# Kernel optimization log

Measured on AMD Instinct MI355X. Metric: run time of the kernel, lower is better.

## Reference

```python
import jax, jax.numpy as jnp
import numpy as np

N = 100000   # nodes
E = 200000   # edges
L = 3        # GNN layers
D = 300      # node feature dim
H = 150      # per-direction message dim


def setup_inputs() -> dict:
    key = jax.random.key(0)
    ks = jax.random.split(key, 8)
    s = 0.05
    return {
        "x": jax.random.normal(ks[0], (N, D), jnp.float32),
        "edge_index": jax.random.randint(ks[1], (2, E), 0, N, dtype=jnp.int32),
        "Wr": jax.random.normal(ks[2], (L, 2 * D, H), jnp.float32) * s,
        "br": jax.random.normal(ks[3], (L, H), jnp.float32) * s,
        "Wc": jax.random.normal(ks[4], (L, 2 * D, H), jnp.float32) * s,
        "bc": jax.random.normal(ks[5], (L, H), jnp.float32) * s,
        "Wa": jax.random.normal(ks[6], (D, D), jnp.float32) * s,
        "ba": jax.random.normal(ks[7], (D,), jnp.float32) * s,
    }


def _gelu(z):
    return jax.nn.gelu(z, approximate=False)  # torch GELU is exact erf


def _msg_aggr(v, src, dst, W, b):
    # message at each edge: GELU(Linear(cat(x_i, x_j))), x_i = target, x_j = source
    m = _gelu(jnp.concatenate([v[dst], v[src]], axis=-1) @ W + b)  # [E, H]
    # sum-aggregate messages at target nodes
    return jax.ops.segment_sum(m, dst, num_segments=N)  # [N, H]


def reference(x, edge_index, Wr, br, Wc, bc, Wa, ba):
    src, dst = edge_index[0], edge_index[1]

    def step(v, p):
        Wr_l, br_l, Wc_l, bc_l = p
        r = _msg_aggr(v, src, dst, Wr_l, br_l)        # r2c: original direction
        c = _msg_aggr(v, dst, src, Wc_l, bc_l)        # c2r: flipped edge_index
        v = v + _gelu(jnp.concatenate([r, c], axis=-1) @ Wa + ba)
        return v, None

    out, _ = jax.lax.scan(step, x, (Wr, br, Wc, bc))
    return out
```

## Files before the change

kernel.cpp:

```cpp
#include <hip/hip_runtime.h>
#include <hip/hip_bf16.h>
#include <math.h>

#define NND 100000
#define EE  200000
#define LL  3
#define DD  300
#define HH  150

#define MPAD 100096
#define KP   320
#define NPJ  640
#define NUP  384
#define NTK  (KP / 32)

#define NB   49
#define SCN  (NB * 2048)

typedef __attribute__((ext_vector_type(8))) short bf16x8;
typedef __attribute__((ext_vector_type(4))) short bf16x4;
typedef __attribute__((ext_vector_type(4))) float f32x4;

__device__ __forceinline__ float gelu_exact(float z) {
    return 0.5f * z * (1.0f + erff(z * 0.7071067811865475f));
}
__device__ __forceinline__ unsigned short f2bf(float f) {
    union { float fv; unsigned u; } v; v.fv = f;
    unsigned r = v.u + 0x7fff + ((v.u >> 16) & 1);
    return (unsigned short)(r >> 16);
}
__device__ __forceinline__ float bf2f(unsigned short b) {
    union { unsigned u; float fv; } v; v.u = ((unsigned)b) << 16;
    return v.fv;
}

__global__ __launch_bounds__(256) void pack_w(
    const float* __restrict__ Wr, const float* __restrict__ Wc,
    const float* __restrict__ Wa,
    unsigned short* __restrict__ Bt, unsigned short* __restrict__ Wat)
{
    int i = blockIdx.x * 256 + threadIdx.x;
    const int btTotal = LL * NPJ * KP;
    if (i < btTotal) {
        int l = i / (NPJ * KP);
        int rem = i % (NPJ * KP);
        int n = rem / KP;
        int k = rem % KP;
        float v = 0.f;
        if (k < DD && n < 600) {
            const float* W = (n < 300) ? Wr : Wc;
            int nn = (n < 300) ? n : n - 300;
            int krow = (nn < 150) ? k : 300 + k;
            int j    = (nn < 150) ? nn : nn - 150;
            v = W[(size_t)l * 600 * 150 + (size_t)krow * 150 + j];
        }
        Bt[i] = f2bf(v);
    } else {
        int i2 = i - btTotal;
        if (i2 < NUP * KP) {
            int n = i2 / KP, k = i2 % KP;
            float v = (n < DD && k < DD) ? Wa[(size_t)k * DD + n] : 0.f;
            Wat[i2] = f2bf(v);
        }
    }
}

__global__ __launch_bounds__(256) void init_vbf(
    const float* __restrict__ x, unsigned short* __restrict__ vbf)
{
    int idx = blockIdx.x * 256 + threadIdx.x;
    int row = idx / (KP / 8);
    int gk  = (idx % (KP / 8)) * 8;
    if (row >= MPAD) return;
    unsigned short tmp[8];
    if (row < NND && gk < DD) {
        if (gk + 8 <= DD) {
            const float4* p = (const float4*)(x + (size_t)row * DD + gk);
            float4 f0 = p[0], f1 = p[1];
            tmp[0] = f2bf(f0.x); tmp[1] = f2bf(f0.y);
            tmp[2] = f2bf(f0.z); tmp[3] = f2bf(f0.w);
            tmp[4] = f2bf(f1.x); tmp[5] = f2bf(f1.y);
            tmp[6] = f2bf(f1.z); tmp[7] = f2bf(f1.w);
        } else {
            #pragma unroll
            for (int j = 0; j < 8; ++j)
                tmp[j] = (gk + j < DD) ? f2bf(x[(size_t)row * DD + gk + j]) : 0;
        }
    } else {
        #pragma unroll
        for (int j = 0; j < 8; ++j) tmp[j] = 0;
    }
    *((bf16x8*)&vbf[(size_t)row * KP + gk]) = *((bf16x8*)tmp);
}

__global__ __launch_bounds__(256) void hist_deg(
    const int* __restrict__ src, const int* __restrict__ dst,
    int* __restrict__ deg)
{
    int e = blockIdx.x * 256 + threadIdx.x;
    if (e >= EE) return;
    atomicAdd(&deg[dst[e]], 1);
    atomicAdd(&deg[SCN + src[e]], 1);
}

__global__ __launch_bounds__(256) void scanA(
    const int* __restrict__ deg, int* __restrict__ off, int* __restrict__ bsum)
{
    __shared__ int ls[256];
    const int t = threadIdx.x, row = blockIdx.y;
    const int base = blockIdx.x * 2048 + t * 8;
    const int* dg = deg + (size_t)row * SCN + base;
    int v[8];
    #pragma unroll
    for (int j = 0; j < 8; ++j) v[j] = dg[j];
    int tot = 0;
    #pragma unroll
    for (int j = 0; j < 8; ++j) tot += v[j];
    ls[t] = tot;
    __syncthreads();
    #pragma unroll
    for (int d = 1; d < 256; d <<= 1) {
        int tv = (t >= d) ? ls[t - d] : 0;
        __syncthreads();
        ls[t] += tv;
        __syncthreads();
    }
    int run = ls[t] - tot;
    int* op = off + (size_t)row * SCN + base;
    #pragma unroll
    for (int j = 0; j < 8; ++j) { op[j] = run; run += v[j]; }
    if (t == 255) bsum[row * 64 + blockIdx.x] = ls[255];
}

__global__ __launch_bounds__(256) void scanB(int* __restrict__ bsum)
{
    if (threadIdx.x < 2) {
        int row = threadIdx.x, c = 0;
        for (int i = 0; i < NB; ++i) {
            int tv = bsum[row * 64 + i];
            bsum[row * 64 + i] = c;
            c += tv;
        }
    }
}

__global__ __launch_bounds__(256) void scanC(
    int* __restrict__ off, const int* __restrict__ bsum, int* __restrict__ cur)
{
    const int t = threadIdx.x, row = blockIdx.y;
    const int base = blockIdx.x * 2048 + t * 8;
    const int add = bsum[row * 64 + blockIdx.x];
    int* op = off + (size_t)row * SCN + base;
    int* cp = cur + (size_t)row * SCN + base;
    #pragma unroll
    for (int j = 0; j < 8; ++j) {
        int v = op[j] + add;
        op[j] = v;
        cp[j] = v;
    }
}

__global__ __launch_bounds__(256) void fill_adj(
    const int* __restrict__ src, const int* __restrict__ dst,
    int* __restrict__ cur, int* __restrict__ adj)
{
    int e = blockIdx.x * 256 + threadIdx.x;
    if (e >= EE) return;
    int s = src[e], d = dst[e];
    int pd = atomicAdd(&cur[d], 1);
    adj[pd] = s;
    int ps = atomicAdd(&cur[SCN + s], 1);
    adj[EE + ps] = d;
}

__global__ __launch_bounds__(256) void aggregate(
    const int* __restrict__ off, const int* __restrict__ adj,
    const unsigned short* __restrict__ P,
    const float* __restrict__ br, const float* __restrict__ bc,
    unsigned short* __restrict__ RC)
{
    const int n    = blockIdx.x * 4 + (threadIdx.x >> 6);
    const int dir  = blockIdx.y;
    const int lane = threadIdx.x & 63;
    const int h0 = lane, h1 = lane + 64, h2 = lane + 128;

    unsigned short* outrow = RC + (size_t)n * KP + dir * 150;
    if (n >= NND) {
        outrow[h0] = 0; outrow[h1] = 0;
        if (h2 < (dir ? 170 : 150)) outrow[h2] = 0;
        return;
    }

    const int* offp = off + (size_t)dir * SCN;
    const int* adjp = adj + (size_t)dir * EE;
    const float* bias = dir ? bc : br;
    const unsigned short* own = P + (size_t)n * NPJ + dir * 300;
    const int poff = dir ? 450 : 150;

    float o0 = bf2f(own[h0]) + bias[h0];
    float o1 = bf2f(own[h1]) + bias[h1];
    float o2 = (h2 < 150) ? bf2f(own[h2]) + bias[h2] : 0.f;

    float s0 = 0.f, s1 = 0.f, s2 = 0.f;
    int beg = offp[n], end = offp[n + 1];
    for (int i = beg; i < end; ++i) {
        const unsigned short* pp = P + (size_t)adjp[i] * NPJ + poff;
        s0 += gelu_exact(o0 + bf2f(pp[h0]));
        s1 += gelu_exact(o1 + bf2f(pp[h1]));
        if (h2 < 150) s2 += gelu_exact(o2 + bf2f(pp[h2]));
    }
    outrow[h0] = f2bf(s0);
    outrow[h1] = f2bf(s1);
    if (h2 < 150)                  outrow[h2] = f2bf(s2);
    else if (dir == 1 && h2 < 170) outrow[h2] = 0;
}

#define GLOAD16(gp, lp) __builtin_amdgcn_global_load_lds( \
    (const __attribute__((address_space(1))) unsigned int*)(gp), \
    (__attribute__((address_space(3))) unsigned int*)(lp), 16, 0, 0)

#define STAGE_LDS(dstp, srcbase, rowoff, k0) do {                            \
    _Pragma("unroll")                                                        \
    for (int i_ = 0; i_ < 2; ++i_) {                                         \
        int cb_ = wid * 128 + i_ * 64;                                       \
        int ci_ = cb_ + lane;                                                \
        int row_ = ci_ >> 2, pc_ = ci_ & 3;                                  \
        int c_ = pc_ ^ ((row_ >> 1) & 3);                                    \
        GLOAD16(srcbase + (size_t)(rowoff + row_) * KP + (k0) + c_ * 8,      \
                &(dstp)[cb_ * 8]);                                           \
    } } while (0)

template<int MODE>
__global__ __launch_bounds__(256) void gemm_mfma(
    const unsigned short* __restrict__ Ab,
    const unsigned short* __restrict__ Bt,
    unsigned short* __restrict__ P,
    float* __restrict__ outv, unsigned short* __restrict__ vbf,
    const float* __restrict__ bias, int last)
{
    __shared__ char smem[49152];
    float* bounce = (float*)smem;

    const int tid  = threadIdx.x;
    const int lane = tid & 63;
    const int wid  = tid >> 6;

    const int gx   = gridDim.x;
    const int nwg  = gx * gridDim.y;
    const int flat = blockIdx.y * gx + blockIdx.x;
    const int q = nwg >> 3, r = nwg & 7;
    const int xcd = flat & 7, off = flat >> 3;
    const int lid = (xcd < r ? xcd * (q + 1) : r * (q + 1) + (xcd - r) * q) + off;
    const int brow = (lid / gx) * 128;
    const int bcol = (lid % gx) * 128;

    const int wm = (wid >> 1) * 64;
    const int wn = (wid & 1) * 64;

    f32x4 acc[4][4];
    #pragma unroll
    for (int i = 0; i < 4; ++i)
        #pragma unroll
        for (int j = 0; j < 4; ++j)
            #pragma unroll
            for (int rr = 0; rr < 4; ++rr) acc[i][j][rr] = 0.f;

    #pragma unroll
    for (int t = 0; t < 2; ++t) {
        unsigned short* Al = (unsigned short*)(smem + t * 16384);
        unsigned short* Bl = (unsigned short*)(smem + t * 16384 + 8192);
        STAGE_LDS(Al, Ab, brow, t * 32);
        STAGE_LDS(Bl, Bt, bcol, t * 32);
    }

    #pragma unroll
    for (int t = 0; t < NTK; ++t) {
        const int b  = t % 3;
        unsigned short* Alc = (unsigned short*)(smem + b * 16384);
        unsigned short* Blc = (unsigned short*)(smem + b * 16384 + 8192);
        if (t + 2 < NTK) {
            const int bn = (t + 2) % 3;
            unsigned short* Aln = (unsigned short*)(smem + bn * 16384);
            unsigned short* Bln = (unsigned short*)(smem + bn * 16384 + 8192);
            STAGE_LDS(Aln, Ab, brow, (t + 2) * 32);
            STAGE_LDS(Bln, Bt, bcol, (t + 2) * 32);
            asm volatile("s_waitcnt vmcnt(8)" ::: "memory");
        } else if (t + 1 < NTK) {
            asm volatile("s_waitcnt vmcnt(4)" ::: "memory");
        } else {
            asm volatile("s_waitcnt vmcnt(0)" ::: "memory");
        }
        __builtin_amdgcn_s_barrier();

        bf16x8 af[4], bfr[4];
        #pragma unroll
        for (int mi = 0; mi < 4; ++mi) {
            int row = wm + mi * 16 + (lane & 15);
            af[mi] = *((const bf16x8*)&Alc[row * 32 + (((lane >> 4) ^ ((row >> 1) & 3)) * 8)]);
        }
        #pragma unroll
        for (int nj = 0; nj < 4; ++nj) {
            int row = wn + nj * 16 + (lane & 15);
            bfr[nj] = *((const bf16x8*)&Blc[row * 32 + (((lane >> 4) ^ ((row >> 1) & 3)) * 8)]);
        }
        __builtin_amdgcn_s_setprio(1);
        #pragma unroll
        for (int mi = 0; mi < 4; ++mi)
            #pragma unroll
            for (int nj = 0; nj < 4; ++nj)
                acc[mi][nj] = __builtin_amdgcn_mfma_f32_16x16x32_bf16(
                    af[mi], bfr[nj], acc[mi][nj], 0, 0, 0);
        __builtin_amdgcn_s_setprio(0);
        __builtin_amdgcn_s_barrier();
    }

    const int ro = tid >> 5;
    const int co = (tid & 31) * 4;
    #pragma unroll
    for (int half = 0; half < 2; ++half) {
        if (wm == half * 64) {
            #pragma unroll
            for (int mi = 0; mi < 4; ++mi)
                #pragma unroll
                for (int nj = 0; nj < 4; ++nj) {
                    int lcol = wn + nj * 16 + (lane & 15);
                    int rb = mi * 16 + ((lane >> 4) << 2);
                    #pragma unroll
                    for (int rr = 0; rr < 4; ++rr)
                        bounce[(rb + rr) * 128 + lcol] = acc[mi][nj][rr];
                }
        }
        __syncthreads();
        #pragma unroll
        for (int i = 0; i < 8; ++i) {
            int lrow = ro + i * 8;
            int grow = brow + half * 64 + lrow;
            float4 vv = *(const float4*)&bounce[lrow * 128 + co];
            if (MODE == 0) {
                bf16x4 o;
                o[0] = (short)f2bf(vv.x); o[1] = (short)f2bf(vv.y);
                o[2] = (short)f2bf(vv.z); o[3] = (short)f2bf(vv.w);
                *((bf16x4*)&P[(size_t)grow * NPJ + bcol + co]) = o;
            } else if (grow < NND) {
                int gc = bcol + co;
                if (bcol < 256) {
                    float4 bv = *(const float4*)&bias[gc];
                    bf16x4 old = *(const bf16x4*)&vbf[(size_t)grow * KP + gc];
                    float4 nv;
                    nv.x = bf2f((unsigned short)old[0]) + gelu_exact(vv.x + bv.x);
                    nv.y = bf2f((unsigned short)old[1]) + gelu_exact(vv.y + bv.y);
                    nv.z = bf2f((unsigned short)old[2]) + gelu_exact(vv.z + bv.z);
                    nv.w = bf2f((unsigned short)old[3]) + gelu_exact(vv.w + bv.w);
                    if (last) {
                        *((float4*)&outv[(size_t)grow * DD + gc]) = nv;
                    } else {
                        bf16x4 o;
                        o[0] = (short)f2bf(nv.x); o[1] = (short)f2bf(nv.y);
                        o[2] = (short)f2bf(nv.z); o[3] = (short)f2bf(nv.w);
                        *((bf16x4*)&vbf[(size_t)grow * KP + gc]) = o;
                    }
                } else {
                    #pragma unroll
                    for (int j = 0; j < 4; ++j) {
                        int c = gc + j;
                        if (c < DD) {
                            float vj = (j == 0) ? vv.x : (j == 1) ? vv.y
                                     : (j == 2) ? vv.z : vv.w;
                            size_t vidx = (size_t)grow * KP + c;
                            float nv = bf2f(vbf[vidx]) + gelu_exact(vj + bias[c]);
                            if (last) outv[(size_t)grow * DD + c] = nv;
                            else      vbf[vidx] = f2bf(nv);
                        }
                    }
                }
            }
        }
        __syncthreads();
    }
}

extern "C" void kernel_launch(void* const* d_in, const int* in_sizes, int n_in,
                              void* d_out, int out_size, void* d_ws, size_t ws_size,
                              hipStream_t stream) {
    const float* x  = (const float*)d_in[0];
    const int*   ei = (const int*)  d_in[1];
    const float* Wr = (const float*)d_in[2];
    const float* br = (const float*)d_in[3];
    const float* Wc = (const float*)d_in[4];
    const float* bc = (const float*)d_in[5];
    const float* Wa = (const float*)d_in[6];
    const float* ba = (const float*)d_in[7];
    float* out = (float*)d_out;

    const size_t P_elems   = (size_t)MPAD * NPJ;
    const size_t RC_elems  = (size_t)MPAD * KP;
    const size_t V_elems   = (size_t)MPAD * KP;
    const size_t Bt_elems  = (size_t)LL * NPJ * KP;
    const size_t Wat_elems = (size_t)NUP * KP;

    unsigned short* P   = (unsigned short*)d_ws;
    unsigned short* RC  = P + P_elems;
    unsigned short* vbf = RC + RC_elems;
    unsigned short* Bt  = vbf + V_elems;
    unsigned short* Wat = Bt + Bt_elems;
    int* deg  = (int*)(Wat + Wat_elems);
    int* off  = deg + 2 * SCN;
    int* curp = off + 2 * SCN;
    int* adj  = curp + 2 * SCN;
    int* bsum = adj + 2 * EE;
    const size_t need = (char*)(bsum + 128) - (char*)d_ws;
    if (ws_size < need) return;

    pack_w<<<2880, 256, 0, stream>>>(Wr, Wc, Wa, Bt, Wat);
    init_vbf<<<(int)((V_elems / 8 + 255) / 256), 256, 0, stream>>>(x, vbf);

    const int* src = ei;
    const int* dst = ei + EE;

    hipMemsetAsync(deg, 0, 2 * SCN * sizeof(int), stream);
    hist_deg<<<(EE + 255) / 256, 256, 0, stream>>>(src, dst, deg);
    scanA<<<dim3(NB, 2), 256, 0, stream>>>(deg, off, bsum);
    scanB<<<1, 256, 0, stream>>>(bsum);
    scanC<<<dim3(NB, 2), 256, 0, stream>>>(off, bsum, curp);
    fill_adj<<<(EE + 255) / 256, 256, 0, stream>>>(src, dst, curp, adj);

    dim3 gproj(NPJ / 128, MPAD / 128);
    dim3 gupd (NUP / 128, MPAD / 128);
    dim3 gagg (MPAD / 4, 2);

    for (int l = 0; l < LL; ++l) {
        gemm_mfma<0><<<gproj, 256, 0, stream>>>(
            vbf, Bt + (size_t)l * NPJ * KP, P, nullptr, nullptr, nullptr, 0);
        aggregate<<<gagg, 256, 0, stream>>>(
            off, adj, P, br + (size_t)l * HH, bc + (size_t)l * HH, RC);
        gemm_mfma<1><<<gupd, 256, 0, stream>>>(
            RC, Wat, nullptr, out, vbf, ba, (l == LL - 1) ? 1 : 0);
    }
}
```

Baseline: 1.030 ms.

## Load GEMM operands directly from global into registers, dropping LDS staging

The MFMA GEMM no longer stages A/B tiles through a triple-buffered LDS pipeline with global_load_lds and barriers. Each wave now loads its bf16x8 fragments straight from global memory into registers every K step. The epilogue bounce buffer is padded to a stride of 132 to avoid LDS bank conflicts. The changes remove barrier and LDS traffic and free LDS for occupancy, but they give up data sharing across waves, so each operand is read twice from global/L2, and there is no explicit prefetch.

```diff
diff --git a/kernel.cpp b/kernel.cpp
--- a/kernel.cpp
+++ b/kernel.cpp
@@ -16,6 +16,8 @@
 
 #define NB   49
 #define SCN  (NB * 2048)
+
+#define BSTRIDE 132
 
 typedef __attribute__((ext_vector_type(8))) short bf16x8;
 typedef __attribute__((ext_vector_type(4))) short bf16x4;
@@ -215,31 +217,15 @@
     else if (dir == 1 && h2 < 170) outrow[h2] = 0;
 }
 
-#define GLOAD16(gp, lp) __builtin_amdgcn_global_load_lds( \
-    (const __attribute__((address_space(1))) unsigned int*)(gp), \
-    (__attribute__((address_space(3))) unsigned int*)(lp), 16, 0, 0)
-
-#define STAGE_LDS(dstp, srcbase, rowoff, k0) do {                            \
-    _Pragma("unroll")                                                        \
-    for (int i_ = 0; i_ < 2; ++i_) {                                         \
-        int cb_ = wid * 128 + i_ * 64;                                       \
-        int ci_ = cb_ + lane;                                                \
-        int row_ = ci_ >> 2, pc_ = ci_ & 3;                                  \
-        int c_ = pc_ ^ ((row_ >> 1) & 3);                                    \
-        GLOAD16(srcbase + (size_t)(rowoff + row_) * KP + (k0) + c_ * 8,      \
-                &(dstp)[cb_ * 8]);                                           \
-    } } while (0)
-
 template<int MODE>
-__global__ __launch_bounds__(256) void gemm_mfma(
+__global__ __launch_bounds__(256) void gemm_dreg(
     const unsigned short* __restrict__ Ab,
     const unsigned short* __restrict__ Bt,
     unsigned short* __restrict__ P,
     float* __restrict__ outv, unsigned short* __restrict__ vbf,
     const float* __restrict__ bias, int last)
 {
-    __shared__ char smem[49152];
-    float* bounce = (float*)smem;
+    __shared__ float bounce[64 * BSTRIDE];
 
     const int tid  = threadIdx.x;
     const int lane = tid & 63;
@@ -254,8 +240,13 @@
     const int brow = (lid / gx) * 128;
     const int bcol = (lid % gx) * 128;
 
-    const int wm = (wid >> 1) * 64;
-    const int wn = (wid & 1) * 64;
+    const int wr = wid >> 1;
+    const int wc = wid & 1;
+
+    const unsigned short* Abase =
+        Ab + (size_t)(brow + wr * 64 + (lane & 15)) * KP + (lane >> 4) * 8;
+    const unsigned short* Bbase =
+        Bt + (size_t)(bcol + wc * 64 + (lane & 15)) * KP + (lane >> 4) * 8;
 
     f32x4 acc[4][4];
     #pragma unroll
@@ -266,68 +257,36 @@
             for (int rr = 0; rr < 4; ++rr) acc[i][j][rr] = 0.f;
 
     #pragma unroll
-    for (int t = 0; t < 2; ++t) {
-        unsigned short* Al = (unsigned short*)(smem + t * 16384);
-        unsigned short* Bl = (unsigned short*)(smem + t * 16384 + 8192);
-        STAGE_LDS(Al, Ab, brow, t * 32);
-        STAGE_LDS(Bl, Bt, bcol, t * 32);
-    }
-
-    #pragma unroll
     for (int t = 0; t < NTK; ++t) {
-        const int b  = t % 3;
-        unsigned short* Alc = (unsigned short*)(smem + b * 16384);
-        unsigned short* Blc = (unsigned short*)(smem + b * 16384 + 8192);
-        if (t + 2 < NTK) {
-            const int bn = (t + 2) % 3;
-            unsigned short* Aln = (unsigned short*)(smem + bn * 16384);
-            unsigned short* Bln = (unsigned short*)(smem + bn * 16384 + 8192);
-            STAGE_LDS(Aln, Ab, brow, (t + 2) * 32);
-            STAGE_LDS(Bln, Bt, bcol, (t + 2) * 32);
-            asm volatile("s_waitcnt vmcnt(8)" ::: "memory");
-        } else if (t + 1 < NTK) {
-            asm volatile("s_waitcnt vmcnt(4)" ::: "memory");
-        } else {
-            asm volatile("s_waitcnt vmcnt(0)" ::: "memory");
-        }
-        __builtin_amdgcn_s_barrier();
-
         bf16x8 af[4], bfr[4];
         #pragma unroll
-        for (int mi = 0; mi < 4; ++mi) {
-            int row = wm + mi * 16 + (lane & 15);
-            af[mi] = *((const bf16x8*)&Alc[row * 32 + (((lane >> 4) ^ ((row >> 1) & 3)) * 8)]);
-        }
-        #pragma unroll
-        for (int nj = 0; nj < 4; ++nj) {
-            int row = wn + nj * 16 + (lane & 15);
-            bfr[nj] = *((const bf16x8*)&Blc[row * 32 + (((lane >> 4) ^ ((row >> 1) & 3)) * 8)]);
-        }
-        __builtin_amdgcn_s_setprio(1);
+        for (int mi = 0; mi < 4; ++mi)
+            af[mi] = *((const bf16x8*)(Abase + (size_t)mi * 16 * KP + t * 32));
+        #pragma unroll
+        for (int nj = 0; nj < 4; ++nj)
+            bfr[nj] = *((const bf16x8*)(Bbase + (size_t)nj * 16 * KP + t * 32));
         #pragma unroll
         for (int mi = 0; mi < 4; ++mi)
             #pragma unroll
             for (int nj = 0; nj < 4; ++nj)
                 acc[mi][nj] = __builtin_amdgcn_mfma_f32_16x16x32_bf16(
                     af[mi], bfr[nj], acc[mi][nj], 0, 0, 0);
-        __builtin_amdgcn_s_setprio(0);
-        __builtin_amdgcn_s_barrier();
     }
 
     const int ro = tid >> 5;
     const int co = (tid & 31) * 4;
     #pragma unroll
     for (int half = 0; half < 2; ++half) {
-        if (wm == half * 64) {
+        if (wr == half) {
             #pragma unroll
             for (int mi = 0; mi < 4; ++mi)
                 #pragma unroll
                 for (int nj = 0; nj < 4; ++nj) {
-                    int lcol = wn + nj * 16 + (lane & 15);
+                    int lcol = wc * 64 + nj * 16 + (lane & 15);
                     int rb = mi * 16 + ((lane >> 4) << 2);
                     #pragma unroll
                     for (int rr = 0; rr < 4; ++rr)
-                        bounce[(rb + rr) * 128 + lcol] = acc[mi][nj][rr];
+                        bounce[(rb + rr) * BSTRIDE + lcol] = acc[mi][nj][rr];
                 }
         }
         __syncthreads();
@@ -335,7 +294,7 @@
         for (int i = 0; i < 8; ++i) {
             int lrow = ro + i * 8;
             int grow = brow + half * 64 + lrow;
-            float4 vv = *(const float4*)&bounce[lrow * 128 + co];
+            float4 vv = *(const float4*)&bounce[lrow * BSTRIDE + co];
             if (MODE == 0) {
                 bf16x4 o;
                 o[0] = (short)f2bf(vv.x); o[1] = (short)f2bf(vv.y);
@@ -429,11 +388,11 @@
     dim3 gagg (MPAD / 4, 2);
 
     for (int l = 0; l < LL; ++l) {
-        gemm_mfma<0><<<gproj, 256, 0, stream>>>(
+        gemm_dreg<0><<<gproj, 256, 0, stream>>>(
             vbf, Bt + (size_t)l * NPJ * KP, P, nullptr, nullptr, nullptr, 0);
         aggregate<<<gagg, 256, 0, stream>>>(
             off, adj, P, br + (size_t)l * HH, bc + (size_t)l * HH, RC);
-        gemm_mfma<1><<<gupd, 256, 0, stream>>>(
+        gemm_dreg<1><<<gupd, 256, 0, stream>>>(
             RC, Wat, nullptr, out, vbf, ba, (l == LL - 1) ? 1 : 0);
     }
 }
```

Result: slower. 1.466 ms (+42.3%).
